# Optimization experiments

Hardware: AMD Instinct MI355X
Metric: run time of the kernel (lower is better)

Reference implementation:

```python
import jax, jax.numpy as jnp
import numpy as np

N = 65536      # tokens
D = 512        # input_dim
H = 8          # num_heads
HD = 64        # head_dim
FF = 2048      # hidden_dim
EPS = 1e-5


def _layer_norm(x, g, b):
    mu = jnp.mean(x, axis=-1, keepdims=True)
    var = jnp.mean(jnp.square(x - mu), axis=-1, keepdims=True)
    return (x - mu) * jax.lax.rsqrt(var + EPS) * g + b


def setup_inputs() -> dict:
    key = jax.random.key(0)
    ks = jax.random.split(key, 12)
    s_d = 1.0 / np.sqrt(D)
    s_f = 1.0 / np.sqrt(FF)
    return {
        "x":   jax.random.normal(ks[0], (N, D), jnp.float32),
        # Linear weights stored [in, out] (transpose of torch's [out, in])
        "Wq":  jax.random.uniform(ks[1], (D, D), jnp.float32, -s_d, s_d),
        "bq":  jnp.zeros((D,), jnp.float32),
        "Wk":  jax.random.uniform(ks[2], (D, D), jnp.float32, -s_d, s_d),
        "bk":  jnp.zeros((D,), jnp.float32),
        "Wv":  jax.random.uniform(ks[3], (D, D), jnp.float32, -s_d, s_d),
        "bv":  jnp.zeros((D,), jnp.float32),
        "ln1_g": jnp.ones((D,), jnp.float32),
        "ln1_b": jnp.zeros((D,), jnp.float32),
        "W1":  jax.random.uniform(ks[4], (D, FF), jnp.float32, -s_d, s_d),
        "b1":  jnp.zeros((FF,), jnp.float32),
        "W2":  jax.random.uniform(ks[5], (FF, D), jnp.float32, -s_f, s_f),
        "b2":  jnp.zeros((D,), jnp.float32),
        "ln2_g": jnp.ones((D,), jnp.float32),
        "ln2_b": jnp.zeros((D,), jnp.float32),
    }


def reference(x, Wq, bq, Wk, bk, Wv, bv, ln1_g, ln1_b, W1, b1, W2, b2, ln2_g, ln2_b):
    n = x.shape[0]
    # --- multi-head attention (per-token head mixing, as in source) ---
    q = (x @ Wq + bq).reshape(n, H, HD)
    k = (x @ Wk + bk).reshape(n, H, HD)
    v = (x @ Wv + bv).reshape(n, H, HD)
    # score[n] = q[n] @ k[n]^T : [H, H] per token
    score = jnp.einsum("nhd,ngd->nhg", q, k) / jnp.sqrt(jnp.float32(HD))
    attn = jax.nn.softmax(score, axis=-1)
    ctx = jnp.einsum("nhg,ngd->nhd", attn, v).reshape(n, D)
    y = _layer_norm(x + ctx, ln1_g, ln1_b)
    # --- feed forward with residual + layer norm ---
    h = jax.nn.relu(y @ W1 + b1)
    z = h @ W2 + b2 + y
    return _layer_norm(z, ln2_g, ln2_b)
```

## Files before the change

kernel.cpp:

```cpp
#include <hip/hip_runtime.h>
#include <cstdint>


typedef __attribute__((ext_vector_type(8))) short bf16x8;
typedef __attribute__((ext_vector_type(4))) float f32x4;
typedef __attribute__((ext_vector_type(8))) unsigned short u16x8;

__device__ __forceinline__ float bf2f(unsigned short u) {
  union { unsigned int i; float f; } v; v.i = ((unsigned int)u) << 16; return v.f;
}
__device__ __forceinline__ unsigned short f2bf(float f) {
  union { float f; unsigned int i; } v; v.f = f;
  unsigned int r = v.i + 0x7FFFu + ((v.i >> 16) & 1u);
  return (unsigned short)(r >> 16);
}

#define GLD16(g, l)                                                         \
  __builtin_amdgcn_global_load_lds(                                         \
      (const __attribute__((address_space(1))) void*)(g),                   \
      (__attribute__((address_space(3))) void*)(l), 16, 0, 0)

__global__ __launch_bounds__(256) void cast_f32_bf16(
    const float* __restrict__ in, ushort* __restrict__ out) {
  const size_t i = (size_t)blockIdx.x * 256 + threadIdx.x;
  const float4* p = (const float4*)in + i * 2;
  float4 a = p[0], b = p[1];
  u16x8 r;
  r[0] = f2bf(a.x); r[1] = f2bf(a.y); r[2] = f2bf(a.z); r[3] = f2bf(a.w);
  r[4] = f2bf(b.x); r[5] = f2bf(b.y); r[6] = f2bf(b.z); r[7] = f2bf(b.w);
  ((u16x8*)out)[i] = r;
}

__global__ __launch_bounds__(256) void transpose_cast(
    const float* __restrict__ W, ushort* __restrict__ Wt,
    int K, int Nn, int rowoff, int ldt) {
  __shared__ float tile[32][33];
  const int tx = threadIdx.x & 31, ty = threadIdx.x >> 5;
  const int nb = blockIdx.x * 32, kb = blockIdx.y * 32;
#pragma unroll
  for (int s = 0; s < 4; ++s)
    tile[ty + 8 * s][tx] = W[(size_t)(kb + ty + 8 * s) * Nn + nb + tx];
  __syncthreads();
#pragma unroll
  for (int s = 0; s < 4; ++s)
    Wt[(size_t)(rowoff + nb + ty + 8 * s) * ldt + kb + tx] =
        f2bf(tile[tx][ty + 8 * s]);
}

template <int EPI>
__global__ __launch_bounds__(512, 2) void gemm_bt(
    const ushort* __restrict__ A, const ushort* __restrict__ Bt,
    int N, int K, void* __restrict__ Cout,
    const float* __restrict__ bias0, const float* __restrict__ bias1,
    const float* __restrict__ bias2, const ushort* __restrict__ resid) {
  constexpr int BK = 32;
  __shared__ __align__(16) ushort lds[2 * 16384];
  const int tid = threadIdx.x;
  const int wid = tid >> 6, lane = tid & 63;
  const int wm = wid >> 2, wn = wid & 3;

  const int gx = gridDim.x;
  const int nwg = gx * gridDim.y;
  const int orig = blockIdx.y * gx + blockIdx.x;
  const int q8 = nwg >> 3, r8 = nwg & 7;
  const int xcd = orig & 7, loc = orig >> 3;
  const int swz = (xcd < r8) ? (xcd * (q8 + 1) + loc)
                             : (r8 * (q8 + 1) + (xcd - r8) * q8 + loc);
  const size_t m0 = (size_t)(swz / gx) * 256;
  const size_t n0 = (size_t)(swz % gx) * 256;
  const int NT = K / BK;

  const int sgcol = (((tid & 3) - ((tid >> 3) & 3)) & 3) << 3;
  const ushort* a0 = A + (m0 + (tid >> 2)) * (size_t)K + sgcol;
  const ushort* b0 = Bt + (n0 + (tid >> 2)) * (size_t)K + sgcol;
  const size_t rowK = 128 * (size_t)K;
  ushort* ldst = &lds[tid * 8];

#define STAGE_SLOT(t, sl)                                                   \
  {                                                                         \
    ushort* d = ldst + ((t) & 1) * 16384 + (sl) * 4096;                     \
    const ushort* g = (((sl) < 2) ? a0 : b0) + (size_t)(t) * BK +           \
                      (((sl) & 1) ? rowK : 0);                              \
    GLD16(g, d);                                                            \
  }

  const int cswz = ((((lane >> 4) + ((lane >> 1) & 3)) & 3) << 3);
  const int arow = wm * 128 + (lane & 15);
  const int brow = wn * 64 + (lane & 15);

  f32x4 acc[8][4] = {};

  STAGE_SLOT(0, 0); STAGE_SLOT(0, 1);
  STAGE_SLOT(0, 2); STAGE_SLOT(0, 3);

  for (int t = 0; t < NT; ++t) {
    asm volatile("s_waitcnt vmcnt(0)" ::: "memory");
    __builtin_amdgcn_s_barrier();

    const ushort* lA = &lds[(t & 1) * 16384];
    const ushort* lB = lA + 8192;

    if (t + 1 < NT) {
      STAGE_SLOT(t + 1, 0); STAGE_SLOT(t + 1, 1);
      STAGE_SLOT(t + 1, 2); STAGE_SLOT(t + 1, 3);
    }

    bf16x8 bfr[4], af[8];
#pragma unroll
    for (int ni = 0; ni < 4; ++ni)
      bfr[ni] = *(const bf16x8*)&lB[(brow + ni * 16) * 32 + cswz];
#pragma unroll
    for (int mi = 0; mi < 8; ++mi)
      af[mi] = *(const bf16x8*)&lA[(arow + mi * 16) * 32 + cswz];

    __builtin_amdgcn_s_setprio(1);
#pragma unroll
    for (int mi = 0; mi < 8; ++mi)
#pragma unroll
      for (int ni = 0; ni < 4; ++ni)
        acc[mi][ni] = __builtin_amdgcn_mfma_f32_16x16x32_bf16(
            af[mi], bfr[ni], acc[mi][ni], 0, 0, 0);
    __builtin_amdgcn_s_setprio(0);
  }
#undef STAGE_SLOT

  const int lm = lane & 15, lq = lane >> 4;
  size_t col[4];
  float bv[4];
#pragma unroll
  for (int ni = 0; ni < 4; ++ni) {
    col[ni] = n0 + wn * 64 + ni * 16 + lm;
    if (EPI == 0) {
      const float* bp = (n0 < 512) ? bias0 : ((n0 < 1024) ? bias1 : bias2);
      bv[ni] = bp[col[ni] & 511];
    } else {
      bv[ni] = bias0[col[ni]];
    }
  }
#pragma unroll
  for (int mi = 0; mi < 8; ++mi) {
#pragma unroll
    for (int j = 0; j < 4; ++j) {
      const size_t row = m0 + wm * 128 + mi * 16 + lq * 4 + j;
#pragma unroll
      for (int ni = 0; ni < 4; ++ni) {
        float v = acc[mi][ni][j] + bv[ni];
        if (EPI == 0) {
          ((ushort*)Cout)[row * N + col[ni]] = f2bf(v);
        } else if (EPI == 1) {
          ((ushort*)Cout)[row * N + col[ni]] = f2bf(fmaxf(v, 0.f));
        } else {
          v += bf2f(resid[row * N + col[ni]]);
          ((ushort*)Cout)[row * N + col[ni]] = f2bf(v);
        }
      }
    }
  }
}

__global__ __launch_bounds__(256) void attn_ln1(
    const ushort* __restrict__ qkv, const ushort* __restrict__ xb,
    const float* __restrict__ g1, const float* __restrict__ b1,
    ushort* __restrict__ y) {
  const int lane = threadIdx.x & 63;
  const size_t t = (size_t)blockIdx.x * 4 + (threadIdx.x >> 6);
  const ushort* base = qkv + t * 1536;
  float qd[8], kd[8], vd[8];
#pragma unroll
  for (int h = 0; h < 8; ++h) {
    qd[h] = bf2f(base[h * 64 + lane]);
    kd[h] = bf2f(base[512 + h * 64 + lane]);
    vd[h] = bf2f(base[1024 + h * 64 + lane]);
  }

  const bool lb0 = lane & 1, lb1 = lane & 2, lb2 = lane & 4;
  const bool lb3 = lane & 8, lb4 = lane & 16, lb5 = lane & 32;

  float c1[32];
#pragma unroll
  for (int f = 0; f < 32; ++f) {
    const int i0 = 2 * f, i1 = 2 * f + 1;
    const float a0 = qd[i0 >> 3] * kd[i0 & 7];
    const float a1 = qd[i1 >> 3] * kd[i1 & 7];
    const float keep = lb0 ? a1 : a0;
    const float send = lb0 ? a0 : a1;
    c1[f] = keep + __shfl_xor(send, 1, 64);
  }
  float c2[16];
#pragma unroll
  for (int f = 0; f < 16; ++f) {
    const float keep = lb1 ? c1[2 * f + 1] : c1[2 * f];
    const float send = lb1 ? c1[2 * f] : c1[2 * f + 1];
    c2[f] = keep + __shfl_xor(send, 2, 64);
  }
  float c3[8];
#pragma unroll
  for (int f = 0; f < 8; ++f) {
    const float keep = lb2 ? c2[2 * f + 1] : c2[2 * f];
    const float send = lb2 ? c2[2 * f] : c2[2 * f + 1];
    c3[f] = keep + __shfl_xor(send, 4, 64);
  }
  float c4[4];
#pragma unroll
  for (int f = 0; f < 4; ++f) {
    const float keep = lb3 ? c3[2 * f + 1] : c3[2 * f];
    const float send = lb3 ? c3[2 * f] : c3[2 * f + 1];
    c4[f] = keep + __shfl_xor(send, 8, 64);
  }
  float c5[2];
#pragma unroll
  for (int f = 0; f < 2; ++f) {
    const float keep = lb4 ? c4[2 * f + 1] : c4[2 * f];
    const float send = lb4 ? c4[2 * f] : c4[2 * f + 1];
    c5[f] = keep + __shfl_xor(send, 16, 64);
  }
  const float keep = lb5 ? c5[1] : c5[0];
  const float send = lb5 ? c5[0] : c5[1];
  const float s = keep + __shfl_xor(send, 32, 64);

  float mx = s;
  mx = fmaxf(mx, __shfl_xor(mx, 1, 64));
  mx = fmaxf(mx, __shfl_xor(mx, 2, 64));
  mx = fmaxf(mx, __shfl_xor(mx, 4, 64));
  const float e = __expf((s - mx) * 0.125f);
  float sum = e;
  sum += __shfl_xor(sum, 1, 64);
  sum += __shfl_xor(sum, 2, 64);
  sum += __shfl_xor(sum, 4, 64);
  const float a = e * __builtin_amdgcn_rcpf(sum);

  const int ai = __float_as_int(a);
  float r[8];
#pragma unroll
  for (int h = 0; h < 8; ++h) {
    float c = 0.f;
#pragma unroll
    for (int g = 0; g < 8; ++g) {
      const float w = __int_as_float(__builtin_amdgcn_readlane(ai, h * 8 + g));
      c = fmaf(w, vd[g], c);
    }
    r[h] = bf2f(xb[t * 512 + h * 64 + lane]) + c;
  }

  float sm = 0.f, sq = 0.f;
#pragma unroll
  for (int h = 0; h < 8; ++h) { sm += r[h]; sq += r[h] * r[h]; }
#pragma unroll
  for (int m = 1; m < 64; m <<= 1) {
    sm += __shfl_xor(sm, m, 64);
    sq += __shfl_xor(sq, m, 64);
  }
  const float mu = sm * (1.f / 512.f);
  const float var = sq * (1.f / 512.f) - mu * mu;
  const float rs = rsqrtf(var + 1e-5f);
#pragma unroll
  for (int h = 0; h < 8; ++h) {
    const int d = h * 64 + lane;
    y[t * 512 + d] = f2bf((r[h] - mu) * rs * g1[d] + b1[d]);
  }
}

__global__ __launch_bounds__(256) void ln_out(
    const ushort* __restrict__ zb, const float* __restrict__ g2,
    const float* __restrict__ b2, float* __restrict__ out) {
  const int lane = threadIdx.x & 63;
  const size_t t = (size_t)blockIdx.x * 4 + (threadIdx.x >> 6);
  const u16x8 v = ((const u16x8*)(zb + t * 512))[lane];
  float r[8];
  float sm = 0.f, sq = 0.f;
#pragma unroll
  for (int j = 0; j < 8; ++j) {
    r[j] = bf2f(v[j]);
    sm += r[j];
    sq += r[j] * r[j];
  }
#pragma unroll
  for (int m = 1; m < 64; m <<= 1) {
    sm += __shfl_xor(sm, m, 64);
    sq += __shfl_xor(sq, m, 64);
  }
  const float mu = sm * (1.f / 512.f);
  const float rs = rsqrtf(sq * (1.f / 512.f) - mu * mu + 1e-5f);
  const int d0 = lane * 8;
  const float4 ga = *(const float4*)(g2 + d0);
  const float4 gb = *(const float4*)(g2 + d0 + 4);
  const float4 ba = *(const float4*)(b2 + d0);
  const float4 bb = *(const float4*)(b2 + d0 + 4);
  float4 oa, ob;
  oa.x = (r[0] - mu) * rs * ga.x + ba.x;
  oa.y = (r[1] - mu) * rs * ga.y + ba.y;
  oa.z = (r[2] - mu) * rs * ga.z + ba.z;
  oa.w = (r[3] - mu) * rs * ga.w + ba.w;
  ob.x = (r[4] - mu) * rs * gb.x + bb.x;
  ob.y = (r[5] - mu) * rs * gb.y + bb.y;
  ob.z = (r[6] - mu) * rs * gb.z + bb.z;
  ob.w = (r[7] - mu) * rs * gb.w + bb.w;
  float* o = out + t * 512 + d0;
  *(float4*)o = oa;
  *(float4*)(o + 4) = ob;
}

extern "C" void kernel_launch(void* const* d_in, const int* in_sizes, int n_in,
                              void* d_out, int out_size, void* d_ws,
                              size_t ws_size, hipStream_t stream) {
  const float* x    = (const float*)d_in[0];
  const float* Wq   = (const float*)d_in[1];
  const float* bq   = (const float*)d_in[2];
  const float* Wk   = (const float*)d_in[3];
  const float* bk   = (const float*)d_in[4];
  const float* Wv   = (const float*)d_in[5];
  const float* bv   = (const float*)d_in[6];
  const float* ln1g = (const float*)d_in[7];
  const float* ln1b = (const float*)d_in[8];
  const float* W1   = (const float*)d_in[9];
  const float* b1   = (const float*)d_in[10];
  const float* W2   = (const float*)d_in[11];
  const float* b2   = (const float*)d_in[12];
  const float* ln2g = (const float*)d_in[13];
  const float* ln2b = (const float*)d_in[14];
  float* out = (float*)d_out;

  const int Ntok = in_sizes[0] / 512;

  char* ws = (char*)d_ws;
  ushort* Wqkvt = (ushort*)ws;
  ushort* W1t   = Wqkvt + (size_t)1536 * 512;
  ushort* W2t   = W1t + (size_t)2048 * 512;
  const size_t woff = ((size_t)1536 * 512 + (size_t)2048 * 512 +
                       (size_t)512 * 2048) * 2;

  size_t avail = (ws_size > woff) ? (ws_size - woff) : 0;
  long long Cll = (long long)(avail / 9216);
  Cll = (Cll / 256) * 256;
  if (Cll > 32768) Cll = 32768;
  if (Cll > Ntok) Cll = Ntok;
  if (Cll < 256) Cll = 256;
  const int C = (int)Cll;

  char* cb = ws + woff;
  ushort* xb  = (ushort*)cb;
  ushort* y   = xb + (size_t)C * 512;
  ushort* qkv = y + (size_t)C * 512;
  ushort* hb  = qkv + (size_t)C * 1536;
  ushort* zb  = qkv;

  transpose_cast<<<dim3(16, 16), dim3(256), 0, stream>>>(Wq, Wqkvt, 512, 512, 0, 512);
  transpose_cast<<<dim3(16, 16), dim3(256), 0, stream>>>(Wk, Wqkvt, 512, 512, 512, 512);
  transpose_cast<<<dim3(16, 16), dim3(256), 0, stream>>>(Wv, Wqkvt, 512, 512, 1024, 512);
  transpose_cast<<<dim3(64, 16), dim3(256), 0, stream>>>(W1, W1t, 512, 2048, 0, 512);
  transpose_cast<<<dim3(16, 64), dim3(256), 0, stream>>>(W2, W2t, 2048, 512, 0, 2048);

  for (int t0 = 0; t0 < Ntok; t0 += C) {
    const int Cc = (Ntok - t0 < C) ? (Ntok - t0) : C;
    const float* xc = x + (size_t)t0 * 512;

    cast_f32_bf16<<<dim3((Cc * 512) / 2048), dim3(256), 0, stream>>>(xc, xb);

    gemm_bt<0><<<dim3(1536 / 256, Cc / 256), dim3(512), 0, stream>>>(
        xb, Wqkvt, 1536, 512, qkv, bq, bk, bv, nullptr);

    attn_ln1<<<dim3(Cc / 4), dim3(256), 0, stream>>>(qkv, xb, ln1g, ln1b, y);

    gemm_bt<1><<<dim3(2048 / 256, Cc / 256), dim3(512), 0, stream>>>(
        y, W1t, 2048, 512, hb, b1, nullptr, nullptr, nullptr);

    gemm_bt<2><<<dim3(512 / 256, Cc / 256), dim3(512), 0, stream>>>(
        hb, W2t, 512, 2048, zb, b2, nullptr, nullptr, y);

    ln_out<<<dim3(Cc / 4), dim3(256), 0, stream>>>(
        zb, ln2g, ln2b, out + (size_t)t0 * 512);
  }
}
```

Before: 652.8 us.

## Fuse FFN2 GEMM with residual add and final LayerNorm in one kernel

Replaces the second FFN GEMM plus the separate LayerNorm kernel with a new ffn2_ln kernel. Each 128-row block computes the full 512-column output, adds bias and residual, and reduces row statistics across the four column-waves through LDS before writing fp32 output directly. This removes the bf16 z round trip through global memory and one launch. The fused kernel uses a triple-buffered LDS pipeline, 1 block per CU and larger per-wave accumulators, which may lower occupancy. attn_ln1 also moves to 512-thread blocks.

```diff
diff --git a/kernel.cpp b/kernel.cpp
--- a/kernel.cpp
+++ b/kernel.cpp
@@ -52,7 +52,7 @@
     const ushort* __restrict__ A, const ushort* __restrict__ Bt,
     int N, int K, void* __restrict__ Cout,
     const float* __restrict__ bias0, const float* __restrict__ bias1,
-    const float* __restrict__ bias2, const ushort* __restrict__ resid) {
+    const float* __restrict__ bias2) {
   constexpr int BK = 32;
   __shared__ __align__(16) ushort lds[2 * 16384];
   const int tid = threadIdx.x;
@@ -147,23 +147,165 @@
         float v = acc[mi][ni][j] + bv[ni];
         if (EPI == 0) {
           ((ushort*)Cout)[row * N + col[ni]] = f2bf(v);
-        } else if (EPI == 1) {
+        } else {
           ((ushort*)Cout)[row * N + col[ni]] = f2bf(fmaxf(v, 0.f));
-        } else {
-          v += bf2f(resid[row * N + col[ni]]);
-          ((ushort*)Cout)[row * N + col[ni]] = f2bf(v);
         }
       }
     }
   }
 }
 
-__global__ __launch_bounds__(256) void attn_ln1(
+__global__ __launch_bounds__(512, 1) void ffn2_ln(
+    const ushort* __restrict__ A,
+    const ushort* __restrict__ Bt,
+    const ushort* __restrict__ resid,
+    const float* __restrict__ b2, const float* __restrict__ g2,
+    const float* __restrict__ be2, float* __restrict__ out) {
+  constexpr int K = 2048, BK = 32, NT = K / BK;
+  constexpr int BUF = 20480;
+  __shared__ __align__(16) ushort lds[3 * BUF];
+  const int tid = threadIdx.x;
+  const int wid = tid >> 6, lane = tid & 63;
+  const int wm = wid >> 2, wn = wid & 3;
+
+  const int nwg = gridDim.x;
+  const int orig = blockIdx.x;
+  const int q8 = nwg >> 3, r8 = nwg & 7;
+  const int xcd = orig & 7, loc = orig >> 3;
+  const int swz = (xcd < r8) ? (xcd * (q8 + 1) + loc)
+                             : (r8 * (q8 + 1) + (xcd - r8) * q8 + loc);
+  const size_t m0 = (size_t)swz * 128;
+
+  const int sgcol = (((tid & 3) - ((tid >> 3) & 3)) & 3) << 3;
+  const ushort* a0 = A + (m0 + (tid >> 2)) * (size_t)K + sgcol;
+  const ushort* b0 = Bt + (tid >> 2) * (size_t)K + sgcol;
+  const size_t rowK128 = 128 * (size_t)K;
+
+#define STAGE_T(t, bi)                                                      \
+  {                                                                         \
+    ushort* da = &lds[(bi) * BUF + tid * 8];                                \
+    GLD16(a0 + (size_t)(t) * BK, da);                                       \
+    const ushort* gb = b0 + (size_t)(t) * BK;                               \
+    ushort* db = &lds[(bi) * BUF + 4096 + tid * 8];                         \
+    GLD16(gb, db);                                                          \
+    GLD16(gb + rowK128, db + 4096);                                         \
+    GLD16(gb + 2 * rowK128, db + 8192);                                     \
+    GLD16(gb + 3 * rowK128, db + 12288);                                    \
+  }
+
+  const int cswz = ((((lane >> 4) + ((lane >> 1) & 3)) & 3) << 3);
+  const int arow = wm * 64 + (lane & 15);
+  const int brow = wn * 128 + (lane & 15);
+
+  f32x4 acc[4][8] = {};
+
+  STAGE_T(0, 0);
+  STAGE_T(1, 1);
+
+  int cur = 0, nx2 = 2;
+  for (int t = 0; t < NT; ++t) {
+    if (t < NT - 1) {
+      asm volatile("s_waitcnt vmcnt(5)" ::: "memory");
+    } else {
+      asm volatile("s_waitcnt vmcnt(0)" ::: "memory");
+    }
+    __builtin_amdgcn_s_barrier();
+
+    const ushort* lA = &lds[cur * BUF];
+    const ushort* lB = lA + 4096;
+
+    if (t + 2 < NT) STAGE_T(t + 2, nx2);
+
+    bf16x8 af[4], bfr[8];
+#pragma unroll
+    for (int ni = 0; ni < 8; ++ni)
+      bfr[ni] = *(const bf16x8*)&lB[(brow + ni * 16) * 32 + cswz];
+#pragma unroll
+    for (int mi = 0; mi < 4; ++mi)
+      af[mi] = *(const bf16x8*)&lA[(arow + mi * 16) * 32 + cswz];
+
+    __builtin_amdgcn_s_setprio(1);
+#pragma unroll
+    for (int mi = 0; mi < 4; ++mi)
+#pragma unroll
+      for (int ni = 0; ni < 8; ++ni)
+        acc[mi][ni] = __builtin_amdgcn_mfma_f32_16x16x32_bf16(
+            af[mi], bfr[ni], acc[mi][ni], 0, 0, 0);
+    __builtin_amdgcn_s_setprio(0);
+
+    cur = (cur == 2) ? 0 : cur + 1;
+    nx2 = (nx2 == 2) ? 0 : nx2 + 1;
+  }
+#undef STAGE_T
+
+  __builtin_amdgcn_s_barrier();
+  float* part = (float*)lds;
+
+  const int lm = lane & 15, lq = lane >> 4;
+  float bcol[8], gcol[8], ecol[8];
+#pragma unroll
+  for (int ni = 0; ni < 8; ++ni) {
+    const int col = wn * 128 + ni * 16 + lm;
+    bcol[ni] = b2[col];
+    gcol[ni] = g2[col];
+    ecol[ni] = be2[col];
+  }
+
+#pragma unroll
+  for (int mi = 0; mi < 4; ++mi) {
+#pragma unroll
+    for (int j = 0; j < 4; ++j) {
+      const size_t row = m0 + wm * 64 + mi * 16 + lq * 4 + j;
+      float s1 = 0.f, s2 = 0.f;
+#pragma unroll
+      for (int ni = 0; ni < 8; ++ni) {
+        const int col = wn * 128 + ni * 16 + lm;
+        float v = acc[mi][ni][j] + bcol[ni] + bf2f(resid[row * 512 + col]);
+        acc[mi][ni][j] = v;
+        s1 += v;
+        s2 += v * v;
+      }
+#pragma unroll
+      for (int m = 1; m < 16; m <<= 1) {
+        s1 += __shfl_xor(s1, m, 64);
+        s2 += __shfl_xor(s2, m, 64);
+      }
+      if (lm == 0) {
+        const int gtok = wm * 64 + mi * 16 + lq * 4 + j;
+        part[(gtok * 4 + wn) * 2 + 0] = s1;
+        part[(gtok * 4 + wn) * 2 + 1] = s2;
+      }
+    }
+  }
+  __builtin_amdgcn_s_barrier();
+
+#pragma unroll
+  for (int mi = 0; mi < 4; ++mi) {
+#pragma unroll
+    for (int j = 0; j < 4; ++j) {
+      const int gtok = wm * 64 + mi * 16 + lq * 4 + j;
+      const float S1 = part[(gtok * 4 + 0) * 2] + part[(gtok * 4 + 1) * 2] +
+                       part[(gtok * 4 + 2) * 2] + part[(gtok * 4 + 3) * 2];
+      const float S2 = part[(gtok * 4 + 0) * 2 + 1] + part[(gtok * 4 + 1) * 2 + 1] +
+                       part[(gtok * 4 + 2) * 2 + 1] + part[(gtok * 4 + 3) * 2 + 1];
+      const float mu = S1 * (1.f / 512.f);
+      const float rs = rsqrtf(S2 * (1.f / 512.f) - mu * mu + 1e-5f);
+      const size_t row = m0 + wm * 64 + mi * 16 + lq * 4 + j;
+#pragma unroll
+      for (int ni = 0; ni < 8; ++ni) {
+        const int col = wn * 128 + ni * 16 + lm;
+        out[row * 512 + col] = (acc[mi][ni][j] - mu) * rs * gcol[ni] + ecol[ni];
+      }
+    }
+  }
+}
+
+__global__ __launch_bounds__(512) void attn_ln1(
     const ushort* __restrict__ qkv, const ushort* __restrict__ xb,
     const float* __restrict__ g1, const float* __restrict__ b1,
     ushort* __restrict__ y) {
   const int lane = threadIdx.x & 63;
-  const size_t t = (size_t)blockIdx.x * 4 + (threadIdx.x >> 6);
+  const size_t t = (size_t)blockIdx.x * 8 + (threadIdx.x >> 6);
   const ushort* base = qkv + t * 1536;
   float qd[8], kd[8], vd[8];
 #pragma unroll
@@ -258,46 +400,6 @@
     const int d = h * 64 + lane;
     y[t * 512 + d] = f2bf((r[h] - mu) * rs * g1[d] + b1[d]);
   }
-}
-
-__global__ __launch_bounds__(256) void ln_out(
-    const ushort* __restrict__ zb, const float* __restrict__ g2,
-    const float* __restrict__ b2, float* __restrict__ out) {
-  const int lane = threadIdx.x & 63;
-  const size_t t = (size_t)blockIdx.x * 4 + (threadIdx.x >> 6);
-  const u16x8 v = ((const u16x8*)(zb + t * 512))[lane];
-  float r[8];
-  float sm = 0.f, sq = 0.f;
-#pragma unroll
-  for (int j = 0; j < 8; ++j) {
-    r[j] = bf2f(v[j]);
-    sm += r[j];
-    sq += r[j] * r[j];
-  }
-#pragma unroll
-  for (int m = 1; m < 64; m <<= 1) {
-    sm += __shfl_xor(sm, m, 64);
-    sq += __shfl_xor(sq, m, 64);
-  }
-  const float mu = sm * (1.f / 512.f);
-  const float rs = rsqrtf(sq * (1.f / 512.f) - mu * mu + 1e-5f);
-  const int d0 = lane * 8;
-  const float4 ga = *(const float4*)(g2 + d0);
-  const float4 gb = *(const float4*)(g2 + d0 + 4);
-  const float4 ba = *(const float4*)(b2 + d0);
-  const float4 bb = *(const float4*)(b2 + d0 + 4);
-  float4 oa, ob;
-  oa.x = (r[0] - mu) * rs * ga.x + ba.x;
-  oa.y = (r[1] - mu) * rs * ga.y + ba.y;
-  oa.z = (r[2] - mu) * rs * ga.z + ba.z;
-  oa.w = (r[3] - mu) * rs * ga.w + ba.w;
-  ob.x = (r[4] - mu) * rs * gb.x + bb.x;
-  ob.y = (r[5] - mu) * rs * gb.y + bb.y;
-  ob.z = (r[6] - mu) * rs * gb.z + bb.z;
-  ob.w = (r[7] - mu) * rs * gb.w + bb.w;
-  float* o = out + t * 512 + d0;
-  *(float4*)o = oa;
-  *(float4*)(o + 4) = ob;
 }
 
 extern "C" void kernel_launch(void* const* d_in, const int* in_sizes, int n_in,
@@ -342,7 +444,6 @@
   ushort* y   = xb + (size_t)C * 512;
   ushort* qkv = y + (size_t)C * 512;
   ushort* hb  = qkv + (size_t)C * 1536;
-  ushort* zb  = qkv;
 
   transpose_cast<<<dim3(16, 16), dim3(256), 0, stream>>>(Wq, Wqkvt, 512, 512, 0, 512);
   transpose_cast<<<dim3(16, 16), dim3(256), 0, stream>>>(Wk, Wqkvt, 512, 512, 512, 512);
@@ -357,17 +458,14 @@
     cast_f32_bf16<<<dim3((Cc * 512) / 2048), dim3(256), 0, stream>>>(xc, xb);
 
     gemm_bt<0><<<dim3(1536 / 256, Cc / 256), dim3(512), 0, stream>>>(
-        xb, Wqkvt, 1536, 512, qkv, bq, bk, bv, nullptr);
-
-    attn_ln1<<<dim3(Cc / 4), dim3(256), 0, stream>>>(qkv, xb, ln1g, ln1b, y);
+        xb, Wqkvt, 1536, 512, qkv, bq, bk, bv);
+
+    attn_ln1<<<dim3(Cc / 8), dim3(512), 0, stream>>>(qkv, xb, ln1g, ln1b, y);
 
     gemm_bt<1><<<dim3(2048 / 256, Cc / 256), dim3(512), 0, stream>>>(
-        y, W1t, 2048, 512, hb, b1, nullptr, nullptr, nullptr);
-
-    gemm_bt<2><<<dim3(512 / 256, Cc / 256), dim3(512), 0, stream>>>(
-        hb, W2t, 512, 2048, zb, b2, nullptr, nullptr, y);
-
-    ln_out<<<dim3(Cc / 4), dim3(256), 0, stream>>>(
-        zb, ln2g, ln2b, out + (size_t)t0 * 512);
-  }
-}
+        y, W1t, 2048, 512, hb, b1, nullptr, nullptr);
+
+    ffn2_ln<<<dim3(Cc / 128), dim3(512), 0, stream>>>(
+        hb, W2t, y, b2, ln2g, ln2b, out + (size_t)t0 * 512);
+  }
+}
```

Result: slower. 675.1 us (+3.4%).
